# Performance work log

Measured on AMD Instinct MI355X. Metric: run time of the kernel, lower is better.

Reference implementation:

```python
import jax, jax.numpy as jnp
import numpy as np
import math

B, L, D = 8, 2048, 1024
DK = D  # self.dk = input_size


def setup_inputs() -> dict:
    key = jax.random.key(0)
    ks = jax.random.split(key, 7)
    s = 1.0 / math.sqrt(D)
    return {
        "x": jax.random.normal(ks[0], (B, L, D), jnp.float32),
        "queries": jax.random.normal(ks[1], (B, L, D), jnp.float32),
        "values": jax.random.normal(ks[2], (B, L, D), jnp.float32),
        "attention_mask": jnp.ones((B, L), jnp.float32),
        "Wk": jax.random.normal(ks[3], (D, D), jnp.float32) * s,
        "Wq_self": jax.random.normal(ks[4], (D, D), jnp.float32) * s,
        "Wq_other": jax.random.normal(ks[5], (D, D), jnp.float32) * s,
        "Wv": jax.random.normal(ks[6], (D, D), jnp.float32) * s,
    }


def reference(x, queries, values, attention_mask, Wk, Wq_self, Wq_other, Wv):
    # nn.Linear(bias=False): y = x @ W.T, weight W is [out, in]
    k = jnp.einsum('bld,ad->bla', x, Wk)
    q_s = jnp.einsum('bld,ad->bla', x, Wq_self)
    q_o = jnp.einsum('bld,ad->bla', queries, Wq_other)
    v = jnp.einsum('bld,ad->bla', values, Wv)

    scale = 1.0 / math.sqrt(DK)
    penalty = (1.0 - attention_mask)[:, None, :] * -100000.0  # (B,1,L)

    scores_self = jnp.einsum('bqa,bka->bqk', q_s, k) * scale + penalty
    scores_other = jnp.einsum('bqa,bka->bqk', q_o, k) * scale + penalty

    p_self = jax.nn.softmax(scores_self, axis=-1)   # dropout is eval/no-op
    p_other = jax.nn.softmax(scores_other, axis=-1)

    out = jnp.einsum('bqk,bka->bqa', p_self, v) + jnp.einsum('bqk,bka->bqa', p_other, v)
    return out, p_self
```

## Files before the change

kernel.cpp:

```cpp
#include <hip/hip_runtime.h>
#include <hip/hip_bf16.h>
#include <cstdint>
#include <cstddef>


#define B_ 8
#define L_ 2048
#define D_ 1024

typedef __attribute__((ext_vector_type(8))) short short8;
typedef __attribute__((ext_vector_type(4))) float floatx4;

__device__ __forceinline__ ushort f2bf(float f) {
  union { float f; uint32_t u; } v; v.f = f;
  return (ushort)((v.u + 0x7FFFu + ((v.u >> 16) & 1u)) >> 16);
}

__device__ __forceinline__ void gload_lds16(const ushort* g, ushort* l) {
  __builtin_amdgcn_global_load_lds(
      (const __attribute__((address_space(1))) void*)g,
      (__attribute__((address_space(3))) void*)l, 16, 0, 0);
}

template<int EPI>
__global__ __launch_bounds__(256) void gemm_bt(
    const ushort* __restrict__ A, long long aBatch, int aStride,
    const ushort* __restrict__ Bm, long long bBatch, int bStride,
    void* __restrict__ Cv, long long cBatch, int cStride,
    int K, const float* __restrict__ mask, int maskStride, float scale)
{
  __shared__ alignas(16) ushort lA[128 * 32];
  __shared__ alignas(16) ushort lB[128 * 32];
  const int tid  = threadIdx.x;
  const int lane = tid & 63;
  const int wave = tid >> 6;
  const int z    = blockIdx.z;

  const ushort* Ab = A + (long long)z * aBatch + (long long)blockIdx.x * 128 * aStride;
  const ushort* Bb = Bm + (long long)z * bBatch + (long long)blockIdx.y * 128 * bStride;

  const int wm = (wave & 1) * 64;
  const int wn = (wave >> 1) * 64;

  const floatx4 zero = {0.f, 0.f, 0.f, 0.f};
  floatx4 acc[4][4];
#pragma unroll
  for (int i = 0; i < 4; i++)
#pragma unroll
    for (int j = 0; j < 4; j++) acc[i][j] = zero;

  for (int k0 = 0; k0 < K; k0 += 32) {
    __syncthreads();
#pragma unroll
    for (int j = 0; j < 2; ++j) {
      int lin = j * 256 + tid;
      int row = lin >> 2;
      int col = (lin & 3) << 3;
      gload_lds16(Ab + (long long)row * aStride + (k0 + col), lA + lin * 8);
      gload_lds16(Bb + (long long)row * bStride + (k0 + col), lB + lin * 8);
    }
    __syncthreads();

    short8 af[4], bg[4];
#pragma unroll
    for (int i = 0; i < 4; i++) {
      af[i] = *(const short8*)(lA + ((wm + i * 16 + (lane & 15)) * 32 + (lane >> 4) * 8));
      bg[i] = *(const short8*)(lB + ((wn + i * 16 + (lane & 15)) * 32 + (lane >> 4) * 8));
    }
#pragma unroll
    for (int i = 0; i < 4; i++)
#pragma unroll
      for (int j = 0; j < 4; j++)
        acc[i][j] = __builtin_amdgcn_mfma_f32_16x16x32_bf16(af[i], bg[j], acc[i][j], 0, 0, 0);
  }

  const int m0 = blockIdx.x * 128 + wm + (lane >> 4) * 4;
  const int n0 = blockIdx.y * 128 + wn + (lane & 15);

  if (EPI == 0) {
    ushort* C = (ushort*)Cv + (long long)z * cBatch;
#pragma unroll
    for (int i = 0; i < 4; i++)
#pragma unroll
      for (int j = 0; j < 4; j++) {
        int gc = n0 + j * 16;
#pragma unroll
        for (int r = 0; r < 4; r++)
          C[(long long)(m0 + i * 16 + r) * cStride + gc] = f2bf(acc[i][j][r]);
      }
  } else {
    float* C = (float*)Cv + (long long)z * cBatch;
#pragma unroll
    for (int j = 0; j < 4; j++) {
      int gc = n0 + j * 16;
      float pen = 0.f;
      if (EPI == 1) pen = (1.0f - mask[(long long)z * maskStride + gc]) * -100000.0f;
#pragma unroll
      for (int i = 0; i < 4; i++)
#pragma unroll
        for (int r = 0; r < 4; r++) {
          float v = acc[i][j][r];
          if (EPI == 1) v = v * scale + pen;
          C[(long long)(m0 + i * 16 + r) * cStride + gc] = v;
        }
    }
  }
}

__global__ __launch_bounds__(256) void transpose_bf16(
    const ushort* __restrict__ V, ushort* __restrict__ Vt)
{
  __shared__ ushort t[64][66];
  const int b = blockIdx.z;
  const int k0 = blockIdx.x * 64;
  const int a0 = blockIdx.y * 64;
  const ushort* Vb = V + (size_t)b * (L_ * D_);
  ushort* Vtb = Vt + (size_t)b * (D_ * L_);
  const int tx = threadIdx.x & 63;
  const int ty = threadIdx.x >> 6;
#pragma unroll
  for (int r = 0; r < 16; ++r) {
    int row = r * 4 + ty;
    t[row][tx] = Vb[(size_t)(k0 + row) * D_ + (a0 + tx)];
  }
  __syncthreads();
#pragma unroll
  for (int r = 0; r < 16; ++r) {
    int row = r * 4 + ty;
    Vtb[(size_t)(a0 + row) * L_ + (k0 + tx)] = t[tx][row];
  }
}

__device__ __forceinline__ float block_red(float v, bool domax, float* red)
{
#pragma unroll
  for (int off = 32; off > 0; off >>= 1) {
    float o = __shfl_xor(v, off, 64);
    v = domax ? fmaxf(v, o) : (v + o);
  }
  __syncthreads();
  if ((threadIdx.x & 63) == 0) red[threadIdx.x >> 6] = v;
  __syncthreads();
  return domax ? fmaxf(fmaxf(red[0], red[1]), fmaxf(red[2], red[3]))
               : (red[0] + red[1] + red[2] + red[3]);
}

__global__ __launch_bounds__(256) void softmax2(float* Sself, float* Sother)
{
  __shared__ float red[4];
  const size_t row = blockIdx.x;
  const int tid = threadIdx.x;
  float* rs = Sself + row * (size_t)L_;
  float* ro = Sother + row * (size_t)L_;

  float vs[8], vo[8];
#pragma unroll
  for (int j = 0; j < 8; j++) vs[j] = rs[tid + j * 256];
#pragma unroll
  for (int j = 0; j < 8; j++) vo[j] = ro[tid + j * 256];

  float ms = -3.0e38f, mo = -3.0e38f;
#pragma unroll
  for (int j = 0; j < 8; j++) { ms = fmaxf(ms, vs[j]); mo = fmaxf(mo, vo[j]); }
  ms = block_red(ms, true, red);
  mo = block_red(mo, true, red);

  float ss = 0.f, so = 0.f;
#pragma unroll
  for (int j = 0; j < 8; j++) {
    vs[j] = __expf(vs[j] - ms); ss += vs[j];
    vo[j] = __expf(vo[j] - mo); so += vo[j];
  }
  ss = block_red(ss, false, red);
  so = block_red(so, false, red);
  const float is = 1.f / ss, io = 1.f / so;

  ushort* rp = (ushort*)ro;
#pragma unroll
  for (int j = 0; j < 8; j++) rs[tid + j * 256] = vs[j] * is;
#pragma unroll
  for (int j = 0; j < 8; j++) rp[tid + j * 256] = f2bf(vs[j] * is + vo[j] * io);
}

__global__ __launch_bounds__(256) void cvt4(
    const float* __restrict__ s0, const float* __restrict__ s1,
    const float* __restrict__ s2, const float* __restrict__ s3,
    ushort* __restrict__ dst, int n4)
{
  const float* s = (blockIdx.z == 0) ? s0 : (blockIdx.z == 1) ? s1
                   : (blockIdx.z == 2) ? s2 : s3;
  ushort* d = dst + (size_t)blockIdx.z * (size_t)n4 * 4;
  const float4* sv = (const float4*)s;
  ushort4* dv = (ushort4*)d;
  for (int i = blockIdx.x * 256 + threadIdx.x; i < n4; i += gridDim.x * 256) {
    float4 f = sv[i];
    ushort4 o; o.x = f2bf(f.x); o.y = f2bf(f.y); o.z = f2bf(f.z); o.w = f2bf(f.w);
    dv[i] = o;
  }
}

extern "C" void kernel_launch(void* const* d_in, const int* in_sizes, int n_in,
                              void* d_out, int out_size, void* d_ws, size_t ws_size,
                              hipStream_t stream)
{
  const float* x    = (const float*)d_in[0];
  const float* qry  = (const float*)d_in[1];
  const float* val  = (const float*)d_in[2];
  const float* mask = (const float*)d_in[3];
  const float* Wk   = (const float*)d_in[4];
  const float* Wqs  = (const float*)d_in[5];
  const float* Wqo  = (const float*)d_in[6];
  const float* Wv   = (const float*)d_in[7];

  const size_t NE = (size_t)B_ * L_ * D_;
  const size_t NW = (size_t)D_ * D_;

  float* out   = (float*)d_out;
  float* pself = out + NE;

  char* ws = (char*)d_ws;
  ushort* xb = (ushort*)ws;
  ushort* qb = xb + NE;
  ushort* vb = qb + NE;
  ushort* W4 = vb + NE;
  float*  sother = (float*)ws;
  ushort* Kb = (ushort*)(ws + (size_t)134217728);
  ushort* Vt = Kb + NE;

  ushort* Qs   = (ushort*)d_out;
  ushort* Qo   = Qs + NE;
  ushort* Vtmp = (ushort*)pself;

  const float scale = 0.03125f;

  cvt4<<<dim3(4096, 1, 3), 256, 0, stream>>>(x, qry, val, nullptr, xb, (int)(NE / 4));
  cvt4<<<dim3(1024, 1, 4), 256, 0, stream>>>(Wk, Wqs, Wqo, Wv, W4, (int)(NW / 4));

  dim3 gp(16384 / 128, 1024 / 128, 1);
  gemm_bt<0><<<gp, 256, 0, stream>>>(xb, 0, D_, W4 + 0 * NW, 0, D_, Kb,   0, D_, D_, nullptr, 0, 1.f);
  gemm_bt<0><<<gp, 256, 0, stream>>>(xb, 0, D_, W4 + 1 * NW, 0, D_, Qs,   0, D_, D_, nullptr, 0, 1.f);
  gemm_bt<0><<<gp, 256, 0, stream>>>(qb, 0, D_, W4 + 2 * NW, 0, D_, Qo,   0, D_, D_, nullptr, 0, 1.f);
  gemm_bt<0><<<gp, 256, 0, stream>>>(vb, 0, D_, W4 + 3 * NW, 0, D_, Vtmp, 0, D_, D_, nullptr, 0, 1.f);

  transpose_bf16<<<dim3(L_ / 64, D_ / 64, B_), 256, 0, stream>>>(Vtmp, Vt);

  dim3 gs(L_ / 128, L_ / 128, B_);
  gemm_bt<1><<<gs, 256, 0, stream>>>(Qs, (long long)L_ * D_, D_, Kb, (long long)L_ * D_, D_,
                                     pself, (long long)L_ * L_, L_, D_, mask, L_, scale);
  gemm_bt<1><<<gs, 256, 0, stream>>>(Qo, (long long)L_ * D_, D_, Kb, (long long)L_ * D_, D_,
                                     sother, (long long)L_ * L_, L_, D_, mask, L_, scale);

  softmax2<<<dim3(B_ * L_, 1, 1), 256, 0, stream>>>(pself, sother);

  dim3 go(L_ / 128, D_ / 128, B_);
  gemm_bt<2><<<go, 256, 0, stream>>>((const ushort*)sother, (long long)L_ * 4096, 4096,
                                     Vt, (long long)D_ * L_, L_,
                                     out, (long long)L_ * D_, D_, L_, nullptr, 0, 1.f);
}
```

Before: 1.009 ms.

## Batch GEMM launches, store scores in bf16, and deepen K-step per sync

Merges the four projection GEMMs into one z-batched launch and the two score GEMMs into one launch with 16 z-slices. Score matrices are now written as bf16 instead of fp32, which halves the score write and read traffic. The softmax reads and writes with vectorized uint4/float4 accesses. The GEMM K loop loads two 32-wide LDS tiles per synchronization, halving barrier count at the cost of doubled shared memory. Rounding scores to bf16 before softmax may reduce accuracy of p_self.

```diff
diff --git a/kernel.cpp b/kernel.cpp
--- a/kernel.cpp
+++ b/kernel.cpp
@@ -15,6 +15,10 @@
   union { float f; uint32_t u; } v; v.f = f;
   return (ushort)((v.u + 0x7FFFu + ((v.u >> 16) & 1u)) >> 16);
 }
+__device__ __forceinline__ float bf2f(ushort u) {
+  union { uint32_t u; float f; } v; v.u = ((uint32_t)u) << 16;
+  return v.f;
+}
 
 __device__ __forceinline__ void gload_lds16(const ushort* g, ushort* l) {
   __builtin_amdgcn_global_load_lds(
@@ -22,22 +26,26 @@
       (__attribute__((address_space(3))) void*)l, 16, 0, 0);
 }
 
-template<int EPI>
+template<int MODE>
 __global__ __launch_bounds__(256) void gemm_bt(
     const ushort* __restrict__ A, long long aBatch, int aStride,
     const ushort* __restrict__ Bm, long long bBatch, int bStride,
     void* __restrict__ Cv, long long cBatch, int cStride,
-    int K, const float* __restrict__ mask, int maskStride, float scale)
-{
-  __shared__ alignas(16) ushort lA[128 * 32];
-  __shared__ alignas(16) ushort lB[128 * 32];
+    int K, const float* __restrict__ mask, float scale)
+{
+  __shared__ alignas(16) ushort lA[2][128 * 32];
+  __shared__ alignas(16) ushort lB[2][128 * 32];
   const int tid  = threadIdx.x;
   const int lane = tid & 63;
   const int wave = tid >> 6;
   const int z    = blockIdx.z;
 
-  const ushort* Ab = A + (long long)z * aBatch + (long long)blockIdx.x * 128 * aStride;
-  const ushort* Bb = Bm + (long long)z * bBatch + (long long)blockIdx.y * 128 * bStride;
+  int asel = z, bsel = z, msel = 0;
+  if (MODE == 0) { asel = (z & 1) + (z == 3); }
+  if (MODE == 1) { bsel = z & 7; msel = z & 7; }
+
+  const ushort* Ab = A + (long long)asel * aBatch + (long long)blockIdx.x * 128 * aStride;
+  const ushort* Bb = Bm + (long long)bsel * bBatch + (long long)blockIdx.y * 128 * bStride;
 
   const int wm = (wave & 1) * 64;
   const int wn = (wave >> 1) * 64;
@@ -49,59 +57,65 @@
 #pragma unroll
     for (int j = 0; j < 4; j++) acc[i][j] = zero;
 
-  for (int k0 = 0; k0 < K; k0 += 32) {
+  const int srow = tid >> 2;
+  const int scol = (tid & 3) << 3;
+
+  for (int k0 = 0; k0 < K; k0 += 64) {
     __syncthreads();
 #pragma unroll
-    for (int j = 0; j < 2; ++j) {
-      int lin = j * 256 + tid;
-      int row = lin >> 2;
-      int col = (lin & 3) << 3;
-      gload_lds16(Ab + (long long)row * aStride + (k0 + col), lA + lin * 8);
-      gload_lds16(Bb + (long long)row * bStride + (k0 + col), lB + lin * 8);
+    for (int h = 0; h < 2; ++h) {
+#pragma unroll
+      for (int j = 0; j < 2; ++j) {
+        int row = srow + j * 64;
+        int l   = (j * 256 + tid) * 8;
+        gload_lds16(Ab + (long long)row * aStride + (k0 + h * 32 + scol), lA[h] + l);
+        gload_lds16(Bb + (long long)row * bStride + (k0 + h * 32 + scol), lB[h] + l);
+      }
     }
     __syncthreads();
 
-    short8 af[4], bg[4];
-#pragma unroll
-    for (int i = 0; i < 4; i++) {
-      af[i] = *(const short8*)(lA + ((wm + i * 16 + (lane & 15)) * 32 + (lane >> 4) * 8));
-      bg[i] = *(const short8*)(lB + ((wn + i * 16 + (lane & 15)) * 32 + (lane >> 4) * 8));
+#pragma unroll
+    for (int h = 0; h < 2; ++h) {
+      short8 af[4], bg[4];
+#pragma unroll
+      for (int i = 0; i < 4; i++) {
+        af[i] = *(const short8*)(lA[h] + ((wm + i * 16 + (lane & 15)) * 32 + (lane >> 4) * 8));
+        bg[i] = *(const short8*)(lB[h] + ((wn + i * 16 + (lane & 15)) * 32 + (lane >> 4) * 8));
+      }
+#pragma unroll
+      for (int i = 0; i < 4; i++)
+#pragma unroll
+        for (int j = 0; j < 4; j++)
+          acc[i][j] = __builtin_amdgcn_mfma_f32_16x16x32_bf16(af[i], bg[j], acc[i][j], 0, 0, 0);
     }
-#pragma unroll
-    for (int i = 0; i < 4; i++)
-#pragma unroll
-      for (int j = 0; j < 4; j++)
-        acc[i][j] = __builtin_amdgcn_mfma_f32_16x16x32_bf16(af[i], bg[j], acc[i][j], 0, 0, 0);
   }
 
   const int m0 = blockIdx.x * 128 + wm + (lane >> 4) * 4;
   const int n0 = blockIdx.y * 128 + wn + (lane & 15);
 
-  if (EPI == 0) {
+  if (MODE == 2) {
+    float* C = (float*)Cv + (long long)z * cBatch;
+#pragma unroll
+    for (int i = 0; i < 4; i++)
+#pragma unroll
+      for (int j = 0; j < 4; j++)
+#pragma unroll
+        for (int r = 0; r < 4; r++)
+          C[(long long)(m0 + i * 16 + r) * cStride + (n0 + j * 16)] = acc[i][j][r];
+  } else {
     ushort* C = (ushort*)Cv + (long long)z * cBatch;
 #pragma unroll
-    for (int i = 0; i < 4; i++)
-#pragma unroll
-      for (int j = 0; j < 4; j++) {
-        int gc = n0 + j * 16;
-#pragma unroll
-        for (int r = 0; r < 4; r++)
-          C[(long long)(m0 + i * 16 + r) * cStride + gc] = f2bf(acc[i][j][r]);
-      }
-  } else {
-    float* C = (float*)Cv + (long long)z * cBatch;
-#pragma unroll
     for (int j = 0; j < 4; j++) {
-      int gc = n0 + j * 16;
+      const int gc = n0 + j * 16;
       float pen = 0.f;
-      if (EPI == 1) pen = (1.0f - mask[(long long)z * maskStride + gc]) * -100000.0f;
+      if (MODE == 1) pen = (1.0f - mask[(long long)msel * L_ + gc]) * -100000.0f;
 #pragma unroll
       for (int i = 0; i < 4; i++)
 #pragma unroll
         for (int r = 0; r < 4; r++) {
           float v = acc[i][j][r];
-          if (EPI == 1) v = v * scale + pen;
-          C[(long long)(m0 + i * 16 + r) * cStride + gc] = v;
+          if (MODE == 1) v = v * scale + pen;
+          C[(long long)(m0 + i * 16 + r) * cStride + gc] = f2bf(v);
         }
     }
   }
@@ -145,19 +159,24 @@
                : (red[0] + red[1] + red[2] + red[3]);
 }
 
-__global__ __launch_bounds__(256) void softmax2(float* Sself, float* Sother)
+__global__ __launch_bounds__(256) void softmax2(
+    const ushort* __restrict__ S, float* __restrict__ pself)
 {
   __shared__ float red[4];
   const size_t row = blockIdx.x;
   const int tid = threadIdx.x;
-  float* rs = Sself + row * (size_t)L_;
-  float* ro = Sother + row * (size_t)L_;
+  const size_t half = (size_t)B_ * L_ * L_;
+
+  const uint4* rs = (const uint4*)(S + row * L_);
+  const uint4* ro = (const uint4*)(S + half + row * L_);
+  uint4 us = rs[tid];
+  uint4 uo = ro[tid];
 
   float vs[8], vo[8];
-#pragma unroll
-  for (int j = 0; j < 8; j++) vs[j] = rs[tid + j * 256];
-#pragma unroll
-  for (int j = 0; j < 8; j++) vo[j] = ro[tid + j * 256];
+  const ushort* ps = (const ushort*)&us;
+  const ushort* po = (const ushort*)&uo;
+#pragma unroll
+  for (int j = 0; j < 8; j++) { vs[j] = bf2f(ps[j]); vo[j] = bf2f(po[j]); }
 
   float ms = -3.0e38f, mo = -3.0e38f;
 #pragma unroll
@@ -175,11 +194,18 @@
   so = block_red(so, false, red);
   const float is = 1.f / ss, io = 1.f / so;
 
-  ushort* rp = (ushort*)ro;
-#pragma unroll
-  for (int j = 0; j < 8; j++) rs[tid + j * 256] = vs[j] * is;
-#pragma unroll
-  for (int j = 0; j < 8; j++) rp[tid + j * 256] = f2bf(vs[j] * is + vo[j] * io);
+  float* pr = pself + row * (size_t)L_ + (size_t)tid * 8;
+  float4 o0, o1;
+  o0.x = vs[0] * is; o0.y = vs[1] * is; o0.z = vs[2] * is; o0.w = vs[3] * is;
+  o1.x = vs[4] * is; o1.y = vs[5] * is; o1.z = vs[6] * is; o1.w = vs[7] * is;
+  ((float4*)pr)[0] = o0;
+  ((float4*)pr)[1] = o1;
+
+  uint4 up;
+  ushort* pp = (ushort*)&up;
+#pragma unroll
+  for (int j = 0; j < 8; j++) pp[j] = f2bf(vs[j] * is + vo[j] * io);
+  ((uint4*)(S + half + row * L_))[tid] = up;
 }
 
 __global__ __launch_bounds__(256) void cvt4(
@@ -214,46 +240,42 @@
 
   const size_t NE = (size_t)B_ * L_ * D_;
   const size_t NW = (size_t)D_ * D_;
-
-  float* out   = (float*)d_out;
-  float* pself = out + NE;
+  const size_t NS = (size_t)B_ * L_ * L_;
+
+  float*  out   = (float*)d_out;
+  float*  pself = out + NE;
+
+  ushort* ob = (ushort*)d_out;
+  ushort* Qs   = ob;
+  ushort* Qo   = ob + NE;
+  ushort* Kb   = ob + 2 * NE;
+  ushort* Vtmp = ob + 3 * NE;
 
   char* ws = (char*)d_ws;
   ushort* xb = (ushort*)ws;
-  ushort* qb = xb + NE;
-  ushort* vb = qb + NE;
-  ushort* W4 = vb + NE;
-  float*  sother = (float*)ws;
-  ushort* Kb = (ushort*)(ws + (size_t)134217728);
-  ushort* Vt = Kb + NE;
-
-  ushort* Qs   = (ushort*)d_out;
-  ushort* Qo   = Qs + NE;
-  ushort* Vtmp = (ushort*)pself;
+  ushort* W4 = xb + 3 * NE;
+  ushort* Sc = (ushort*)ws;
+  ushort* Psum = Sc + NS;
+  ushort* Vt = (ushort*)(ws + (size_t)134217728);
 
   const float scale = 0.03125f;
 
   cvt4<<<dim3(4096, 1, 3), 256, 0, stream>>>(x, qry, val, nullptr, xb, (int)(NE / 4));
-  cvt4<<<dim3(1024, 1, 4), 256, 0, stream>>>(Wk, Wqs, Wqo, Wv, W4, (int)(NW / 4));
-
-  dim3 gp(16384 / 128, 1024 / 128, 1);
-  gemm_bt<0><<<gp, 256, 0, stream>>>(xb, 0, D_, W4 + 0 * NW, 0, D_, Kb,   0, D_, D_, nullptr, 0, 1.f);
-  gemm_bt<0><<<gp, 256, 0, stream>>>(xb, 0, D_, W4 + 1 * NW, 0, D_, Qs,   0, D_, D_, nullptr, 0, 1.f);
-  gemm_bt<0><<<gp, 256, 0, stream>>>(qb, 0, D_, W4 + 2 * NW, 0, D_, Qo,   0, D_, D_, nullptr, 0, 1.f);
-  gemm_bt<0><<<gp, 256, 0, stream>>>(vb, 0, D_, W4 + 3 * NW, 0, D_, Vtmp, 0, D_, D_, nullptr, 0, 1.f);
+  cvt4<<<dim3(1024, 1, 4), 256, 0, stream>>>(Wqs, Wqo, Wk, Wv, W4, (int)(NW / 4));
+
+  gemm_bt<0><<<dim3(128, 8, 4), 256, 0, stream>>>(
+      xb, (long long)NE, D_, W4, (long long)NW, D_,
+      ob, (long long)NE, D_, D_, nullptr, 1.f);
 
   transpose_bf16<<<dim3(L_ / 64, D_ / 64, B_), 256, 0, stream>>>(Vtmp, Vt);
 
-  dim3 gs(L_ / 128, L_ / 128, B_);
-  gemm_bt<1><<<gs, 256, 0, stream>>>(Qs, (long long)L_ * D_, D_, Kb, (long long)L_ * D_, D_,
-                                     pself, (long long)L_ * L_, L_, D_, mask, L_, scale);
-  gemm_bt<1><<<gs, 256, 0, stream>>>(Qo, (long long)L_ * D_, D_, Kb, (long long)L_ * D_, D_,
-                                     sother, (long long)L_ * L_, L_, D_, mask, L_, scale);
-
-  softmax2<<<dim3(B_ * L_, 1, 1), 256, 0, stream>>>(pself, sother);
-
-  dim3 go(L_ / 128, D_ / 128, B_);
-  gemm_bt<2><<<go, 256, 0, stream>>>((const ushort*)sother, (long long)L_ * 4096, 4096,
-                                     Vt, (long long)D_ * L_, L_,
-                                     out, (long long)L_ * D_, D_, L_, nullptr, 0, 1.f);
-}
+  gemm_bt<1><<<dim3(16, 16, 16), 256, 0, stream>>>(
+      Qs, (long long)L_ * D_, D_, Kb, (long long)L_ * D_, D_,
+      Sc, (long long)L_ * L_, L_, D_, mask, scale);
+
+  softmax2<<<dim3(B_ * L_, 1, 1), 256, 0, stream>>>(Sc, pself);
+
+  gemm_bt<2><<<dim3(16, 8, 8), 256, 0, stream>>>(
+      Psum, (long long)L_ * L_, L_, Vt, (long long)D_ * L_, L_,
+      out, (long long)L_ * D_, D_, L_, nullptr, 1.f);
+}
```

Measured after the change: 888.6 us. -11.9%, faster.
